# Performance work log

Hardware: AMD Instinct MI355X
Metric: run time of the kernel (lower is better)

The kernel has to match this reference:

```python
import jax, jax.numpy as jnp
import numpy as np

PH, PW = 7, 7          # pooled_height, pooled_width
SCALE = 0.0625         # spatial_scale
K = 6                  # static max integer cells per bin side (max bin size = 448*SCALE/7 = 4)


def setup_inputs() -> dict:
    key = jax.random.key(0)
    kf, kb, kx, ky, kw, kh = jax.random.split(key, 6)
    B, C, H, W = 4, 256, 64, 64
    R = 1024
    features = jax.random.normal(kf, (B, C, H, W), dtype=jnp.float32)
    # rois rows: (batch_idx, x1, y1, x2, y2) in image coords (image ~1024px, scale 1/16)
    bidx = jax.random.randint(kb, (R,), 0, B).astype(jnp.float32)
    x1 = jax.random.uniform(kx, (R,), minval=0.0, maxval=576.0)
    y1 = jax.random.uniform(ky, (R,), minval=0.0, maxval=576.0)
    bw = jax.random.uniform(kw, (R,), minval=32.0, maxval=448.0)
    bh = jax.random.uniform(kh, (R,), minval=32.0, maxval=448.0)
    rois = jnp.stack([bidx, x1, y1, x1 + bw, y1 + bh], axis=1)
    return {"features": features, "rois": rois}


def _gather(features, b, hidx, widx, H, W):
    # hidx: [R,PH] int32, widx: [R,PW] int32 -> [R,PH,PW,C]; out-of-bounds reads are zero
    vh = (hidx >= 0) & (hidx < H)
    vw = (widx >= 0) & (widx < W)
    mask = (vh[:, :, None] & vw[:, None, :]).astype(features.dtype)  # [R,PH,PW]
    hc = jnp.clip(hidx, 0, H - 1)
    wc = jnp.clip(widx, 0, W - 1)
    d = features[b[:, None, None], :, hc[:, :, None], wc[:, None, :]]  # [R,PH,PW,C]
    return d * mask[..., None]


def _cell_weights(start, end, s):
    # exact integrals of the two 1D bilinear hat weights over [start,end] clipped to cell [s, s+1]
    y0 = jnp.maximum(start, s)
    yl = jnp.maximum(jnp.minimum(end, s + 1.0), y0)  # empty intersection -> zero weights
    a = y0 - s
    la = yl - s
    g0 = la - 0.5 * la * la - a + 0.5 * a * a  # weight of node at s
    g1 = 0.5 * la * la - 0.5 * a * a           # weight of node at s+1
    return g0, g1


def prroi_pool(features, rois):
    B, C, H, W = features.shape
    R = rois.shape[0]
    dt = features.dtype
    b = rois[:, 0].astype(jnp.int32)
    x1 = rois[:, 1] * SCALE
    y1 = rois[:, 2] * SCALE
    x2 = rois[:, 3] * SCALE
    y2 = rois[:, 4] * SCALE
    roi_w = jnp.maximum(x2 - x1, 0.0)
    roi_h = jnp.maximum(y2 - y1, 0.0)
    bin_w = roi_w / PW
    bin_h = roi_h / PH
    # per-bin continuous windows [ws, we)
    ws_w = x1[:, None] + bin_w[:, None] * jnp.arange(PW, dtype=dt)  # [R,PW]
    ws_h = y1[:, None] + bin_h[:, None] * jnp.arange(PH, dtype=dt)  # [R,PH]
    we_w = ws_w + bin_w[:, None]
    we_h = ws_h + bin_h[:, None]
    s0_w = jnp.floor(ws_w)
    s0_h = jnp.floor(ws_h)

    offs = np.stack(np.meshgrid(np.arange(K), np.arange(K), indexing="ij"), -1).reshape(-1, 2)
    offs = jnp.asarray(offs, dtype=dt)  # [K*K, 2] (dh, dw)

    def step(acc, off):
        sh = s0_h + off[0]  # [R,PH] float (integer-valued)
        sw = s0_w + off[1]  # [R,PW]
        gy0, gy1 = _cell_weights(ws_h, we_h, sh)
        gx0, gx1 = _cell_weights(ws_w, we_w, sw)
        hi = sh.astype(jnp.int32)
        wi = sw.astype(jnp.int32)
        d00 = _gather(features, b, hi, wi, H, W)
        d01 = _gather(features, b, hi, wi + 1, H, W)
        d10 = _gather(features, b, hi + 1, wi, H, W)
        d11 = _gather(features, b, hi + 1, wi + 1, H, W)
        gy0 = gy0[:, :, None, None]
        gy1 = gy1[:, :, None, None]
        gx0 = gx0[:, None, :, None]
        gx1 = gx1[:, None, :, None]
        contrib = d00 * (gy0 * gx0) + d01 * (gy0 * gx1) + d10 * (gy1 * gx0) + d11 * (gy1 * gx1)
        return acc + contrib, None

    acc0 = jnp.zeros((R, PH, PW, C), dtype=dt)
    acc, _ = jax.lax.scan(step, acc0, offs)
    win = (bin_w * bin_h)[:, None, None, None]  # bin area in feature coords
    out = jnp.where(win > 0, acc / jnp.where(win > 0, win, 1.0), 0.0)
    return jnp.transpose(out, (0, 3, 1, 2))  # [R, C, PH, PW]


def reference(features, rois):
    return prroi_pool(features, rois)
```

## Files before the change

kernel.cpp:

```cpp
#include <hip/hip_runtime.h>
#include <hip/hip_fp16.h>

#define R_    1024
#define B_    4
#define C_    256
#define H_    64
#define W_    64
#define HW_   4096
#define PHW_  49
#define ROIT  128
#define LROWH 130
#define SLACKH 17408

__device__ __forceinline__ void cell_w(float start, float end, float s, float& g0, float& g1) {
    float y0 = fmaxf(start, s);
    float yl = fmaxf(fminf(end, s + 1.0f), y0);
    float a  = y0 - s;
    float la = yl - s;
    g0 = la - 0.5f * la * la - a + 0.5f * a * a;
    g1 = 0.5f * la * la - 0.5f * a * a;
}

__global__ __launch_bounds__(256) void prep(const float* __restrict__ in,
                                            __half* __restrict__ fTh,
                                            const float* __restrict__ rois,
                                            int* __restrict__ perm,
                                            float* __restrict__ roitab) {
    int bid = blockIdx.x;
    if (bid < 4096) {
        __shared__ float tile[32][33];
        int b   = bid >> 10;
        int rem = bid & 1023;
        int c0  = (rem >> 7) * 32;
        int p0  = (rem & 127) * 32;
        int tx  = threadIdx.x & 31;
        int ty  = threadIdx.x >> 5;
        const float* src = in + (size_t)b * C_ * HW_;
#pragma unroll
        for (int i = 0; i < 32; i += 8)
            tile[ty + i][tx] = src[(size_t)(c0 + ty + i) * HW_ + (p0 + tx)];
        __syncthreads();
        __half2* dsth = (__half2*)(fTh + (size_t)b * HW_ * C_);
#pragma unroll
        for (int i = 0; i < 2; ++i) {
            int idx = threadIdx.x + i * 256;
            int py  = idx >> 4;
            int cp  = idx & 15;
            float lo = tile[cp * 2][py];
            float hi = tile[cp * 2 + 1][py];
            dsth[(size_t)(p0 + py) * (C_ / 2) + (c0 >> 1) + cp] = __floats2half2_rn(lo, hi);
        }
        return;
    }
    if (bid == 4096) {
        if (threadIdx.x >= 64) {
            for (int j = threadIdx.x - 64; j < SLACKH; j += 192)
                fTh[(size_t)B_ * HW_ * C_ + j] = __half(0.0f);
            return;
        }
        int lane = threadIdx.x;
        unsigned long long below = (1ull << lane) - 1ull;
        int key[16];
#pragma unroll
        for (int i = 0; i < 16; ++i) {
            int idx = i * 64 + lane;
            const float* roi = rois + idx * 5;
            int b = (int)roi[0];
            float yc = (roi[2] + roi[4]) * 0.5f * 0.0625f;
            int yb = min(3, max(0, (int)(yc * 0.0625f)));
            key[i] = b * 4 + yb;
        }
        int cntk[16];
#pragma unroll
        for (int k = 0; k < 16; ++k) cntk[k] = 0;
        for (int i = 0; i < 16; ++i)
#pragma unroll
            for (int k = 0; k < 16; ++k)
                cntk[k] += __popcll(__ballot(key[i] == k));
        int off[16]; int acc = 0;
#pragma unroll
        for (int k = 0; k < 16; ++k) { off[k] = acc; acc += cntk[k]; }
        for (int i = 0; i < 16; ++i) {
#pragma unroll
            for (int k = 0; k < 16; ++k) {
                unsigned long long m = __ballot(key[i] == k);
                if (key[i] == k)
                    perm[off[k] + __popcll(m & below)] = i * 64 + lane;
                off[k] += __popcll(m);
            }
        }
        return;
    }
    int i = (bid - 4097) * 256 + threadIdx.x;
    int r  = i / PHW_;
    int k  = i - r * PHW_;
    int ph = k / 7, pw = k - ph * 7;
    const float* roi = rois + r * 5;
    int bb = (int)roi[0];
    float x1 = roi[1] * 0.0625f, y1 = roi[2] * 0.0625f;
    float x2 = roi[3] * 0.0625f, y2 = roi[4] * 0.0625f;
    float rw = fmaxf(x2 - x1, 0.0f), rh = fmaxf(y2 - y1, 0.0f);
    float bw = rw / 7.0f, bh = rh / 7.0f;
    float win = bw * bh;
    float* rt = roitab + (size_t)r * ROIT;

    float wy[8], wx[7];
#pragma unroll
    for (int t = 0; t < 7; ++t) { wy[t] = 0.0f; wx[t] = 0.0f; }
    wy[7] = 0.0f;
    int w0 = 0, h0 = 0, npy = 0, w00 = 0;
    float invwin = 0.0f;
    if (win > 0.0f) {
        float ws = x1 + bw * (float)pw, we = ws + bw;
        float hs = y1 + bh * (float)ph, he = hs + bh;
        float s0w = floorf(ws), s0h = floorf(hs);
        w0 = (int)s0w; h0 = (int)s0h;
        w00 = (int)floorf(x1);
#pragma unroll
        for (int o = 0; o < 6; ++o) {
            float g0, g1;
            cell_w(hs, he, s0h + (float)o, g0, g1);
            wy[o] += g0; wy[o + 1] += g1;
            cell_w(ws, we, s0w + (float)o, g0, g1);
            wx[o] += g0; wx[o + 1] += g1;
        }
        npy = min(7, max(0, (int)ceilf(he - s0h + 1.0f)));
        int npx = min(7, max(0, (int)ceilf(we - s0w + 1.0f)));
        npy = max(0, min(npy, H_ - h0));
        npx = max(0, min(npx, W_ - w0));
#pragma unroll
        for (int t = 0; t < 7; ++t) {
            if (t >= npx) wx[t] = 0.0f;
            if (t >= npy) wy[t] = 0.0f;
        }
        invwin = 1.0f / win;
    }
    if (ph == 0) {
#pragma unroll
        for (int t = 0; t < 7; ++t) rt[pw * 7 + t] = wx[t];
        rt[49 + pw] = __int_as_float(w0 - w00);
    }
    if (pw == 0) {
#pragma unroll
        for (int t = 0; t < 8; ++t) rt[72 + ph * 8 + t] = wy[t] * invwin;
        rt[64 + ph] = __int_as_float(h0 | (npy << 8));
    }
    if (k == 0) {
        int jlim = 0;
        if (win > 0.0f) {
#pragma unroll
            for (int p = 0; p < 7; ++p) {
                float wsp = x1 + bw * (float)p, wep = wsp + bw;
                float s0wp = floorf(wsp);
                int w0p = (int)s0wp;
                int npxp = min(7, max(0, (int)ceilf(wep - s0wp + 1.0f)));
                npxp = max(0, min(npxp, W_ - w0p));
                jlim = max(jlim, (w0p - w00) + npxp);
            }
        }
        rt[63] = __int_as_float(bb | (w00 << 8) | (jlim << 16));
    }
}

__global__ __launch_bounds__(256) void prroi_rows(const __half* __restrict__ fTh,
                                                  const int* __restrict__ perm,
                                                  const float* __restrict__ roitab,
                                                  __half* __restrict__ scr) {
    __shared__ __align__(16) float colw[4][32 * 8];
    int wid  = __builtin_amdgcn_readfirstlane(threadIdx.x >> 6);
    int lane = threadIdx.x & 63;
    float* cwv = colw[wid];
    int bid = blockIdx.x;
    int xcd = bid & 7;
    int s   = (bid >> 3) * 4 + wid;
    if (s >= 896) return;
    int t   = (s & 31) * 28 + (s >> 5);
    int g   = xcd * 896 + t;
    int rs  = g / 7;
    int ph  = g - rs * 7;
    int r   = __builtin_amdgcn_readfirstlane(perm[rs]);
    const float* rt = roitab + (size_t)r * ROIT;

#pragma unroll
    for (int u = 0; u < 4; ++u) cwv[lane + u * 64] = 0.0f;
    if (lane < 49) {
        int pw = lane / 7;
        int dx = lane - pw * 7;
        float wxv = rt[lane];
        int d = __float_as_int(rt[49 + pw]);
        cwv[(d + dx) * 8 + pw] = wxv;
    }
    int meta = __float_as_int(rt[63]);
    int bb   = meta & 0xff;
    int w00  = (meta >> 8) & 0xff;
    int jlim = (meta >> 16) & 0xff;
    int hm   = __float_as_int(rt[64 + ph]);
    int h0   = hm & 0xff;
    int npy  = (hm >> 8) & 0xff;
    int npy2 = (npy + 1) & ~1;
    const float* wyp = rt + 72 + ph * 8;

    int half = lane >> 5;
    int cl   = lane & 31;
    const __half* fr = fTh + ((size_t)bb * HW_ + (size_t)h0 * W_ + w00 + half) * C_ + cl * 8;

    float4 aA[7], aB[7];
#pragma unroll
    for (int p = 0; p < 7; ++p) {
        aA[p] = make_float4(0.f, 0.f, 0.f, 0.f);
        aB[p] = make_float4(0.f, 0.f, 0.f, 0.f);
    }

    for (int jl = 0; jl < jlim; jl += 2) {
        const float* cw = cwv + (jl + half) * 8;
        float4 c0 = *(const float4*)(cw);
        float4 c1 = *(const float4*)(cw + 4);
        const __half* cp = fr + (size_t)jl * C_;
        __half2 g0 = __float2half2_rn(0.0f), g1 = g0, g2 = g0, g3 = g0;
        for (int dy = 0; dy < npy2; dy += 2) {
            const __half* r0 = cp + (size_t)dy * (W_ * C_);
            uint4 va = *(const uint4*)(r0);
            uint4 vb = *(const uint4*)(r0 + W_ * C_);
            __half2 w0h = __float2half2_rn(wyp[dy]);
            __half2 w1h = __float2half2_rn(wyp[dy + 1]);
            g0 = __hfma2(w0h, *(__half2*)&va.x, g0);
            g1 = __hfma2(w0h, *(__half2*)&va.y, g1);
            g2 = __hfma2(w0h, *(__half2*)&va.z, g2);
            g3 = __hfma2(w0h, *(__half2*)&va.w, g3);
            g0 = __hfma2(w1h, *(__half2*)&vb.x, g0);
            g1 = __hfma2(w1h, *(__half2*)&vb.y, g1);
            g2 = __hfma2(w1h, *(__half2*)&vb.z, g2);
            g3 = __hfma2(w1h, *(__half2*)&vb.w, g3);
        }
        float2 t0 = __half22float2(g0);
        float2 t1 = __half22float2(g1);
        float2 t2 = __half22float2(g2);
        float2 t3 = __half22float2(g3);
        float4 gA = make_float4(t0.x, t0.y, t1.x, t1.y);
        float4 gB = make_float4(t2.x, t2.y, t3.x, t3.y);
#define APPLY(P, CP) { \
    aA[P].x = fmaf(CP, gA.x, aA[P].x); aA[P].y = fmaf(CP, gA.y, aA[P].y); \
    aA[P].z = fmaf(CP, gA.z, aA[P].z); aA[P].w = fmaf(CP, gA.w, aA[P].w); \
    aB[P].x = fmaf(CP, gB.x, aB[P].x); aB[P].y = fmaf(CP, gB.y, aB[P].y); \
    aB[P].z = fmaf(CP, gB.z, aB[P].z); aB[P].w = fmaf(CP, gB.w, aB[P].w); }
        APPLY(0, c0.x); APPLY(1, c0.y); APPLY(2, c0.z); APPLY(3, c0.w);
        APPLY(4, c1.x); APPLY(5, c1.y); APPLY(6, c1.z);
#undef APPLY
    }

#pragma unroll
    for (int p = 0; p < 7; ++p) {
        aA[p].x += __shfl_xor(aA[p].x, 32);
        aA[p].y += __shfl_xor(aA[p].y, 32);
        aA[p].z += __shfl_xor(aA[p].z, 32);
        aA[p].w += __shfl_xor(aA[p].w, 32);
        aB[p].x += __shfl_xor(aB[p].x, 32);
        aB[p].y += __shfl_xor(aB[p].y, 32);
        aB[p].z += __shfl_xor(aB[p].z, 32);
        aB[p].w += __shfl_xor(aB[p].w, 32);
    }

    __half* sb = scr + ((size_t)r * PHW_ + ph * 7) * C_ + cl * 8;
#pragma unroll
    for (int s4 = 0; s4 < 4; ++s4) {
        const int ihi = (4 + s4 > 6) ? 6 : 4 + s4;
        float4 pa = half ? aA[ihi] : aA[s4];
        float4 pb = half ? aB[ihi] : aB[s4];
        int p = half ? 4 + s4 : s4;
        if (p < 7) {
            union { __half2 h2[4]; uint4 u; } pk;
            pk.h2[0] = __floats2half2_rn(pa.x, pa.y);
            pk.h2[1] = __floats2half2_rn(pa.z, pa.w);
            pk.h2[2] = __floats2half2_rn(pb.x, pb.y);
            pk.h2[3] = __floats2half2_rn(pb.z, pb.w);
            *(uint4*)(sb + (size_t)p * C_) = pk.u;
        }
    }
}

__global__ __launch_bounds__(256) void fixup(const int* __restrict__ perm,
                                             const __half* __restrict__ scr,
                                             float* __restrict__ out) {
    __shared__ __align__(4) __half lds_h[PHW_ * LROWH];
    int bid  = blockIdx.x;
    int idx  = (bid & 7) * 256 + (bid >> 3);
    int rs   = idx >> 1;
    int half = idx & 1;
    int r    = perm[rs];
    const unsigned int* src = (const unsigned int*)(scr + (size_t)r * PHW_ * C_ + half * 128);
    for (int j = threadIdx.x; j < PHW_ * 64; j += 256) {
        int row = j >> 6;
        int col = j & 63;
        *(unsigned int*)&lds_h[row * LROWH + col * 2] = src[(size_t)row * (C_ / 2) + col];
    }
    __syncthreads();
    float* outr = out + (size_t)r * (C_ * PHW_) + (size_t)half * 128 * PHW_;
#pragma unroll 4
    for (int j = threadIdx.x; j < 128 * PHW_; j += 256) {
        int c = j / PHW_;
        int k = j - c * PHW_;
        outr[j] = __half2float(lds_h[k * LROWH + c]);
    }
}

__global__ __launch_bounds__(256) void prroi_pool_direct(const float* __restrict__ f,
                                                         const float* __restrict__ rois,
                                                         float* __restrict__ out) {
    int bin = blockIdx.x;
    int r  = bin / PHW_;
    int k  = bin - r * PHW_;
    int ph = k / 7;
    int pw = k - ph * 7;
    int c = threadIdx.x;

    const float* roi = rois + r * 5;
    int bb = (int)roi[0];
    float x1 = roi[1] * 0.0625f, y1 = roi[2] * 0.0625f;
    float x2 = roi[3] * 0.0625f, y2 = roi[4] * 0.0625f;
    float rw = fmaxf(x2 - x1, 0.0f), rh = fmaxf(y2 - y1, 0.0f);
    float bw = rw / 7.0f, bh = rh / 7.0f;
    float win = bw * bh;
    size_t oidx = ((size_t)r * C_ + c) * PHW_ + k;
    if (!(win > 0.0f)) { out[oidx] = 0.0f; return; }

    float ws = x1 + bw * (float)pw, we = ws + bw;
    float hs = y1 + bh * (float)ph, he = hs + bh;
    float s0w = floorf(ws), s0h = floorf(hs);
    int w0 = (int)s0w, h0 = (int)s0h;
    float wy[7], wx[7];
#pragma unroll
    for (int t = 0; t < 7; ++t) { wy[t] = 0.0f; wx[t] = 0.0f; }
#pragma unroll
    for (int o = 0; o < 6; ++o) {
        float g0, g1;
        cell_w(hs, he, s0h + (float)o, g0, g1);
        wy[o] += g0; wy[o + 1] += g1;
        cell_w(ws, we, s0w + (float)o, g0, g1);
        wx[o] += g0; wx[o + 1] += g1;
    }
    int npy = min(7, max(0, (int)ceilf(he - s0h + 1.0f)));
    int npx = min(7, max(0, (int)ceilf(we - s0w + 1.0f)));
    npy = max(0, min(npy, H_ - h0));
    npx = max(0, min(npx, W_ - w0));

    const float* fbc = f + ((size_t)bb * C_ + c) * (H_ * W_);
    float acc = 0.0f;
#pragma unroll
    for (int dy = 0; dy < 7; ++dy) {
        if (dy < npy) {
            float row = 0.0f;
#pragma unroll
            for (int dx = 0; dx < 7; ++dx) {
                if (dx < npx)
                    row = fmaf(wx[dx], fbc[(h0 + dy) * W_ + (w0 + dx)], row);
            }
            acc = fmaf(wy[dy], row, acc);
        }
    }
    out[oidx] = acc / win;
}

extern "C" void kernel_launch(void* const* d_in, const int* in_sizes, int n_in,
                              void* d_out, int out_size, void* d_ws, size_t ws_size,
                              hipStream_t stream) {
    const float* feat = (const float*)d_in[0];
    const float* rois = (const float*)d_in[1];
    float* out = (float*)d_out;

    const size_t fth_b   = (size_t)B_ * HW_ * C_ * sizeof(__half);
    const size_t slack_b = (size_t)SLACKH * sizeof(__half);
    const size_t perm_b  = (size_t)R_ * sizeof(int);
    const size_t rt_b    = (size_t)R_ * ROIT * sizeof(float);
    const size_t scr_b   = (size_t)R_ * PHW_ * C_ * sizeof(__half);

    const size_t base = fth_b + slack_b + perm_b + rt_b;
    if (ws_size >= base + scr_b) {
        __half* fTh  = (__half*)d_ws;
        int*    perm = (int*)((char*)d_ws + fth_b + slack_b);
        float*  rtab = (float*)((char*)d_ws + fth_b + slack_b + perm_b);
        __half* scr  = (__half*)((char*)d_ws + base);
        prep<<<4293, 256, 0, stream>>>(feat, fTh, rois, perm, rtab);
        prroi_rows<<<2048, 256, 0, stream>>>(fTh, perm, rtab, scr);
        fixup<<<2048, 256, 0, stream>>>(perm, scr, out);
    } else {
        prroi_pool_direct<<<R_ * PHW_, 256, 0, stream>>>(feat, rois, out);
    }
}
```

Before: 61.21 us.

## Widen transpose blocks to full channel rows and prefetch next row pair

The NCHW-to-NHWC half-precision transpose in prep now has each block handle all 256 channels for 32 pixels. It stages half values in a padded LDS tile and writes 8-byte vectors per thread, which cuts the transpose grid from 4096 blocks to 512. The inner vertical accumulation loop in the row kernel is software-pipelined, loading the next pair of feature rows before doing the FMAs on the current pair, to hide global load latency. The cost is fewer, larger transpose blocks with more LDS, plus extra registers for the prefetched vectors. The pipelined loop always runs at least one row-pair iteration, which assumes npy2 is at least 2.

```diff
diff --git a/kernel.cpp b/kernel.cpp
--- a/kernel.cpp
+++ b/kernel.cpp
@@ -10,6 +10,7 @@
 #define PHW_  49
 #define ROIT  128
 #define LROWH 130
+#define TROW  260
 #define SLACKH 17408
 
 __device__ __forceinline__ void cell_w(float start, float end, float s, float& g0, float& g1) {
@@ -27,32 +28,30 @@
                                             int* __restrict__ perm,
                                             float* __restrict__ roitab) {
     int bid = blockIdx.x;
-    if (bid < 4096) {
-        __shared__ float tile[32][33];
-        int b   = bid >> 10;
-        int rem = bid & 1023;
-        int c0  = (rem >> 7) * 32;
-        int p0  = (rem & 127) * 32;
-        int tx  = threadIdx.x & 31;
-        int ty  = threadIdx.x >> 5;
-        const float* src = in + (size_t)b * C_ * HW_;
-#pragma unroll
-        for (int i = 0; i < 32; i += 8)
-            tile[ty + i][tx] = src[(size_t)(c0 + ty + i) * HW_ + (p0 + tx)];
+    if (bid < 512) {
+        __shared__ __align__(16) __half lds_t[32 * TROW];
+        int b  = bid >> 7;
+        int p0 = (bid & 127) * 32;
+        int tx = threadIdx.x & 31;
+        int ty = threadIdx.x >> 5;
+        const float* src = in + (size_t)b * C_ * HW_ + p0 + tx;
+#pragma unroll
+        for (int i = 0; i < 32; ++i) {
+            int c = ty * 32 + i;
+            lds_t[tx * TROW + c] = __float2half(src[(size_t)c * HW_]);
+        }
         __syncthreads();
-        __half2* dsth = (__half2*)(fTh + (size_t)b * HW_ * C_);
-#pragma unroll
-        for (int i = 0; i < 2; ++i) {
-            int idx = threadIdx.x + i * 256;
-            int py  = idx >> 4;
-            int cp  = idx & 15;
-            float lo = tile[cp * 2][py];
-            float hi = tile[cp * 2 + 1][py];
-            dsth[(size_t)(p0 + py) * (C_ / 2) + (c0 >> 1) + cp] = __floats2half2_rn(lo, hi);
+#pragma unroll
+        for (int u = 0; u < 8; ++u) {
+            int e = threadIdx.x + u * 256;
+            int p = e >> 6;
+            int q = e & 63;
+            uint2 v = *(const uint2*)&lds_t[p * TROW + q * 4];
+            *(uint2*)(fTh + ((size_t)b * HW_ + p0 + p) * C_ + q * 4) = v;
         }
         return;
     }
-    if (bid == 4096) {
+    if (bid == 512) {
         if (threadIdx.x >= 64) {
             for (int j = threadIdx.x - 64; j < SLACKH; j += 192)
                 fTh[(size_t)B_ * HW_ * C_ + j] = __half(0.0f);
@@ -91,7 +90,7 @@
         }
         return;
     }
-    int i = (bid - 4097) * 256 + threadIdx.x;
+    int i = (bid - 513) * 256 + threadIdx.x;
     int r  = i / PHW_;
     int k  = i - r * PHW_;
     int ph = k / 7, pw = k - ph * 7;
@@ -217,10 +216,26 @@
         float4 c1 = *(const float4*)(cw + 4);
         const __half* cp = fr + (size_t)jl * C_;
         __half2 g0 = __float2half2_rn(0.0f), g1 = g0, g2 = g0, g3 = g0;
-        for (int dy = 0; dy < npy2; dy += 2) {
-            const __half* r0 = cp + (size_t)dy * (W_ * C_);
-            uint4 va = *(const uint4*)(r0);
-            uint4 vb = *(const uint4*)(r0 + W_ * C_);
+        uint4 va = *(const uint4*)(cp);
+        uint4 vb = *(const uint4*)(cp + W_ * C_);
+        int dy = 0;
+        for (; dy + 2 < npy2; dy += 2) {
+            const __half* rn = cp + (size_t)(dy + 2) * (W_ * C_);
+            uint4 na = *(const uint4*)(rn);
+            uint4 nb = *(const uint4*)(rn + W_ * C_);
+            __half2 w0h = __float2half2_rn(wyp[dy]);
+            __half2 w1h = __float2half2_rn(wyp[dy + 1]);
+            g0 = __hfma2(w0h, *(__half2*)&va.x, g0);
+            g1 = __hfma2(w0h, *(__half2*)&va.y, g1);
+            g2 = __hfma2(w0h, *(__half2*)&va.z, g2);
+            g3 = __hfma2(w0h, *(__half2*)&va.w, g3);
+            g0 = __hfma2(w1h, *(__half2*)&vb.x, g0);
+            g1 = __hfma2(w1h, *(__half2*)&vb.y, g1);
+            g2 = __hfma2(w1h, *(__half2*)&vb.z, g2);
+            g3 = __hfma2(w1h, *(__half2*)&vb.w, g3);
+            va = na; vb = nb;
+        }
+        {
             __half2 w0h = __float2half2_rn(wyp[dy]);
             __half2 w1h = __float2half2_rn(wyp[dy + 1]);
             g0 = __hfma2(w0h, *(__half2*)&va.x, g0);
@@ -379,7 +394,7 @@
         int*    perm = (int*)((char*)d_ws + fth_b + slack_b);
         float*  rtab = (float*)((char*)d_ws + fth_b + slack_b + perm_b);
         __half* scr  = (__half*)((char*)d_ws + base);
-        prep<<<4293, 256, 0, stream>>>(feat, fTh, rois, perm, rtab);
+        prep<<<709, 256, 0, stream>>>(feat, fTh, rois, perm, rtab);
         prroi_rows<<<2048, 256, 0, stream>>>(fTh, perm, rtab, scr);
         fixup<<<2048, 256, 0, stream>>>(perm, scr, out);
     } else {
```

Result: faster. 59.55 us (-2.7%).
